# Optimization experiments

Measured on AMD Instinct MI355X. Metric: run time of the kernel, lower is better.

The kernel has to match this reference:

```python
import jax, jax.numpy as jnp
import numpy as np

N_TOKEN = 100000
D = 1024  # d_embed == d_model == d_proj
CUTOFFS = [0, 20000, 60000, 100000]  # cutoff_ends
N_SEQ = 2048


def setup_inputs() -> dict:
    key = jax.random.key(0)
    ks = jax.random.split(key, 20)
    w = lambda k, s: jax.random.normal(k, s, dtype=jnp.float32) * 0.02
    return {
        "x": jax.random.randint(ks[0], (N_SEQ,), 0, N_TOKEN),
        "labels": jax.random.randint(ks[1], (N_SEQ,), 0, N_TOKEN),
        # adaptive embedding tables (d_emb_i = 1024 / 4**i) and projections [d_proj, d_emb_i]
        "emb_w0": w(ks[2], (20000, 1024)),
        "emb_w1": w(ks[3], (40000, 256)),
        "emb_w2": w(ks[4], (40000, 64)),
        "emb_proj0": w(ks[5], (1024, 1024)),
        "emb_proj1": w(ks[6], (1024, 256)),
        "emb_proj2": w(ks[7], (1024, 64)),
        # adaptive softmax output layers + projections
        "out_w0": w(ks[8], (20000, 1024)),
        "out_b0": jnp.zeros((20000,), jnp.float32),
        "out_w1": w(ks[9], (40000, 256)),
        "out_b1": jnp.zeros((40000,), jnp.float32),
        "out_w2": w(ks[10], (40000, 64)),
        "out_b2": jnp.zeros((40000,), jnp.float32),
        "out_proj0": w(ks[11], (1024, 1024)),
        "out_proj1": w(ks[12], (1024, 256)),
        "out_proj2": w(ks[13], (1024, 64)),
        # cluster head tokens (one per tail cluster)
        "cluster_w": w(ks[14], (2, 1024)),
        "cluster_b": jnp.zeros((2,), jnp.float32),
    }


def _forward(x, labels,
             emb_w0, emb_w1, emb_w2, emb_proj0, emb_proj1, emb_proj2,
             out_w0, out_b0, out_w1, out_b1, out_w2, out_b2,
             out_proj0, out_proj1, out_proj2, cluster_w, cluster_b):
    scale = jnp.asarray(D ** 0.5, jnp.float32)
    # AdaptiveEmbedding (div_val>1): per-cluster embed -> project to d_proj, scatter by range.
    # Equivalent vectorized form: build the full projected table once, then gather.
    table = jnp.concatenate([
        emb_w0 @ emb_proj0.T,   # [20000, D]
        emb_w1 @ emb_proj1.T,   # [40000, D]
        emb_w2 @ emb_proj2.T,   # [40000, D]
    ], axis=0)                   # [N_TOKEN, D]
    hidden = table[x] * scale    # [N, D]

    n = hidden.shape[0]
    rows = jnp.arange(n)

    # Head: cluster-0 vocab + one logit per tail cluster.
    head_w = jnp.concatenate([out_w0, cluster_w], axis=0)   # [20002, D]
    head_b = jnp.concatenate([out_b0, cluster_b], axis=0)   # [20002]
    head_logit = (hidden @ out_proj0) @ head_w.T + head_b   # [N, 20002]
    head_lp = jax.nn.log_softmax(head_logit, axis=-1)
    head_size = head_lp.shape[1]

    # Cluster 0: direct lookup in the head.
    lp0 = head_lp[rows, jnp.clip(labels, 0, CUTOFFS[1] - 1)]

    # Tail clusters: dense per-cluster log-softmax, gathered at shifted target,
    # plus the head cluster-token logprob (original TXL uses column -i).
    def tail(w, b, proj, i):
        l, r = CUTOFFS[i], CUTOFFS[i + 1]
        tail_lp = jax.nn.log_softmax((hidden @ proj) @ w.T + b, axis=-1)  # [N, r-l]
        t = jnp.clip(labels - l, 0, r - l - 1)
        return head_lp[:, head_size - i] + tail_lp[rows, t]

    lp1 = tail(out_w1, out_b1, out_proj1, 1)
    lp2 = tail(out_w2, out_b2, out_proj2, 2)

    logprob = jnp.where(labels < CUTOFFS[1], lp0,
               jnp.where(labels < CUTOFFS[2], lp1, lp2))
    return -logprob  # nll, [N]


def reference(x, labels,
              emb_w0, emb_w1, emb_w2, emb_proj0, emb_proj1, emb_proj2,
              out_w0, out_b0, out_w1, out_b1, out_w2, out_b2,
              out_proj0, out_proj1, out_proj2, cluster_w, cluster_b):
    return _forward(x, labels,
                    emb_w0, emb_w1, emb_w2, emb_proj0, emb_proj1, emb_proj2,
                    out_w0, out_b0, out_w1, out_b1, out_w2, out_b2,
                    out_proj0, out_proj1, out_proj2, cluster_w, cluster_b)
```

## Files before the change

### kernel.cpp

```cpp
#include <hip/hip_runtime.h>

typedef _Float16 f16x8 __attribute__((ext_vector_type(8)));
typedef _Float16 f16x4 __attribute__((ext_vector_type(4)));
typedef float f32x4 __attribute__((ext_vector_type(4)));
typedef int i32x4 __attribute__((ext_vector_type(4)));
typedef int i32x8 __attribute__((ext_vector_type(8)));
typedef unsigned char u8;

#define DEVI __device__ __forceinline__

constexpr int NROWS = 2048;
constexpr int HEADV = 20002;
constexpr int HEADP = 20480;
constexpr int NCBH  = 160;
constexpr int VT    = 40000;
constexpr int VTP   = 40320;
constexpr int NCBT  = 315;

DEVI void glds16(const void* g, void* l) {
  __builtin_amdgcn_global_load_lds((const __attribute__((address_space(1))) unsigned int*)g,
                                   (__attribute__((address_space(3))) unsigned int*)l,
                                   16, 0, 0);
}

#define SIG(r) ((r) & 7)
DEVI int swzb(int b, int r) {
  return (b & ~127) | ((((b >> 4) & 7) ^ SIG(r)) << 4) | (b & 15);
}

DEVI unsigned int to_e4m3(float f) {
  unsigned u = __float_as_uint(f);
  unsigned s = (u >> 24) & 0x80u;
  float a = fabsf(f);
  if (!(a < 448.f)) return s | 0x7E;
  if (a < 0.00097656f) return s;
  int exp = (int)((u >> 23) & 0xFF) - 127;
  int qexp = exp < -6 ? -6 : exp;
  int n = __float2int_rn(a * exp2f((float)(3 - qexp)));
  if (n >= 16) { qexp++; n = 8; }
  return s | (unsigned)(n < 8 ? n : (((qexp + 7) << 3) | (n - 8)));
}

DEVI float fr8(unsigned b) {
  unsigned e = (b >> 3) & 15u, m = b & 7u;
  float v;
  if (e) v = __uint_as_float(((e + 120u) << 23) | (m << 20));
  else   v = (float)m * 0.001953125f;
  return (b & 0x80u) ? -v : v;
}

__global__ void prep_par(const int* __restrict__ x, const int* __restrict__ labels,
                         int* cl, int* headcol, int* tailpos, int* pos1, int* pos2,
                         int* L1, int* L2, int* T0, int* T1, int* T2, int* counts)
{
  int n = blockIdx.x * 256 + threadIdx.x;
  int l = labels[n];
  int c = l < 20000 ? 0 : (l < 60000 ? 1 : 2);
  cl[n] = c;
  headcol[n] = c == 0 ? l : (c == 1 ? 20001 : 20000);
  tailpos[n] = c == 1 ? l - 20000 : (c == 2 ? l - 60000 : 0);
  if (c == 1) { int s = atomicAdd(&counts[0], 1); pos1[n] = s; L1[s] = n; }
  else if (c == 2) { int s = atomicAdd(&counts[1], 1); pos2[n] = s; L2[s] = n; }
  int t = x[n];
  int tc = t < 20000 ? 0 : (t < 60000 ? 1 : 2);
  int s = atomicAdd(&counts[2 + tc], 1);
  (tc == 0 ? T0 : tc == 1 ? T1 : T2)[s] = n;
}

constexpr int PB_A = HEADP * 1024 / 8 / 256;
constexpr int PB_B = PB_A + VTP * 256 / 8 / 256;
constexpr int PB_C = PB_B + VTP * 128 / 8 / 256;
constexpr int PB_D = PB_C + 1024;
constexpr int PB_E = PB_D + 256;
constexpr int PB_F = PB_E + 64;
constexpr int PB_G = PB_F + 1024;
constexpr int PB_H = PB_G + 256;
constexpr int PB_I = PB_H + 128;

DEVI void cvt_f16(const float* src, _Float16* dst, int vb, int tid) {
  int g = vb * 256 + tid;
  float4 v = *(const float4*)(src + (size_t)g * 4);
  f16x4 o = {(_Float16)v.x, (_Float16)v.y, (_Float16)v.z, (_Float16)v.w};
  *(f16x4*)(dst + (size_t)g * 4) = o;
}

DEVI void tr32(const float* in, _Float16* out, int C, int bx, int by, int tid) {
  __shared__ float tile[32][33];
  int c0 = bx * 32, r0 = by * 32;
  int tx = tid & 31, ty = tid >> 5;
  for (int i = 0; i < 4; i++) {
    int c = c0 + tx; int r = r0 + ty + i * 8;
    tile[ty + i * 8][tx] = (c < C) ? in[(size_t)r * C + c] : 0.f;
  }
  __syncthreads();
  for (int i = 0; i < 4; i++)
    out[(size_t)(c0 + ty + i * 8) * 1024 + r0 + tx] = (_Float16)tile[tx][ty + i * 8];
}

DEVI unsigned long pack8(const float* v) {
  unsigned long p = 0;
  #pragma unroll
  for (int j = 0; j < 8; j++) p |= (unsigned long)to_e4m3(v[j] * 64.f) << (8 * j);
  return p;
}

__global__ void fused_pack(const float* __restrict__ out_w0, const float* __restrict__ out_b0,
                           const float* __restrict__ cluster_w, const float* __restrict__ cluster_b,
                           const float* __restrict__ out_w1, const float* __restrict__ out_b1,
                           const float* __restrict__ out_w2, const float* __restrict__ out_b2,
                           const float* __restrict__ emb_proj0, const float* __restrict__ emb_proj1,
                           const float* __restrict__ emb_proj2,
                           const float* __restrict__ out_proj0, const float* __restrict__ out_proj1,
                           const float* __restrict__ out_proj2,
                           u8* headw, float* headb,
                           u8* w1q, float* b1p, u8* w2q, float* b2p,
                           _Float16* ep0f, _Float16* ep1f, _Float16* ep2f,
                           _Float16* op0T, _Float16* op1T, _Float16* op2T,
                           int* lists, int* counts)
{
  int bid = blockIdx.x, tid = threadIdx.x;
  int zi = bid * 256 + tid;
  if (zi < 5 * 2048) lists[zi] = 0;
  if (bid == 41 && tid < 8) counts[tid] = 0;
  if (bid < PB_A) {
    int g = bid * 256 + tid;
    int r = g >> 7, sl = g & 127;
    float v[8] = {};
    if (r < 20000) {
      *(float4*)v = *(const float4*)(out_w0 + (size_t)r * 1024 + sl * 8);
      *(float4*)(v + 4) = *(const float4*)(out_w0 + (size_t)r * 1024 + sl * 8 + 4);
    } else if (r < 20002) {
      *(float4*)v = *(const float4*)(cluster_w + (size_t)(r - 20000) * 1024 + sl * 8);
      *(float4*)(v + 4) = *(const float4*)(cluster_w + (size_t)(r - 20000) * 1024 + sl * 8 + 4);
    }
    *(unsigned long*)(headw + (size_t)r * 1024 + swzb(sl * 8, r)) = pack8(v);
    if (g < HEADP) headb[g] = g < 20000 ? out_b0[g] : (g < HEADV ? cluster_b[g - 20000] : -1e30f);
  } else if (bid < PB_B) {
    int g = (bid - PB_A) * 256 + tid;
    int r = g >> 5, sl = g & 31;
    float v[8] = {};
    if (r < VT) {
      *(float4*)v = *(const float4*)(out_w1 + (size_t)r * 256 + sl * 8);
      *(float4*)(v + 4) = *(const float4*)(out_w1 + (size_t)r * 256 + sl * 8 + 4);
    }
    *(unsigned long*)(w1q + (size_t)r * 256 + swzb(sl * 8, r)) = pack8(v);
    if (g < VTP) b1p[g] = g < VT ? out_b1[g] : -1e30f;
  } else if (bid < PB_C) {
    int g = (bid - PB_B) * 256 + tid;
    int r = g >> 4, sl = g & 15;
    float v[8] = {};
    if (r < VT && sl < 8) {
      *(float4*)v = *(const float4*)(out_w2 + (size_t)r * 64 + sl * 8);
      *(float4*)(v + 4) = *(const float4*)(out_w2 + (size_t)r * 64 + sl * 8 + 4);
    }
    *(unsigned long*)(w2q + (size_t)r * 128 + swzb(sl * 8, r)) = pack8(v);
    if (g < VTP) b2p[g] = g < VT ? out_b2[g] : -1e30f;
  } else if (bid < PB_D) { cvt_f16(emb_proj0, ep0f, bid - PB_C, tid); }
  else if (bid < PB_E) { cvt_f16(emb_proj1, ep1f, bid - PB_D, tid); }
  else if (bid < PB_F) { cvt_f16(emb_proj2, ep2f, bid - PB_E, tid); }
  else if (bid < PB_G) { int l = bid - PB_F; tr32(out_proj0, op0T, 1024, l & 31, l >> 5, tid); }
  else if (bid < PB_H) { int l = bid - PB_G; tr32(out_proj1, op1T, 256, l & 7, l >> 3, tid); }
  else                 { int l = bid - PB_H; tr32(out_proj2, op2T, 64, l & 3, l >> 2, tid); }
}

DEVI void gat(const float* emb, const int* x, const int* list, _Float16* dst,
              int tbase, int vmax, int log2E, int vb, int tid) {
  int g = vb * 256 + tid;
  int r = g >> (log2E - 2);
  int e4 = (g & ((1 << (log2E - 2)) - 1)) << 2;
  int n = list[r];
  int tl = x[n] - tbase;
  tl = tl < 0 ? 0 : (tl >= vmax ? vmax - 1 : tl);
  float4 v = *(const float4*)(emb + ((size_t)tl << log2E) + e4);
  f16x4 o = {(_Float16)(v.x * 32.f), (_Float16)(v.y * 32.f),
             (_Float16)(v.z * 32.f), (_Float16)(v.w * 32.f)};
  *(f16x4*)(dst + ((size_t)r << log2E) + e4) = o;
}

__global__ void fused_gather(const float* __restrict__ emb_w0, const float* __restrict__ emb_w1,
                             const float* __restrict__ emb_w2, const int* __restrict__ x,
                             const int* __restrict__ T0, const int* __restrict__ T1,
                             const int* __restrict__ T2,
                             _Float16* E0, _Float16* E1, _Float16* E2)
{
  int bid = blockIdx.x, tid = threadIdx.x;
  if (bid < 2048)      gat(emb_w0, x, T0, E0, 0, 20000, 10, bid, tid);
  else if (bid < 2560) gat(emb_w1, x, T1, E1, 20000, 40000, 8, bid - 2048, tid);
  else                 gat(emb_w2, x, T2, E2, 60000, 40000, 6, bid - 2560, tid);
}

struct Seg128 {
  const _Float16* A; int lda;
  const _Float16* Wm; int ldw;
  _Float16* C; int ldc; int Nvalid;
  u8* Cq; int ldq;
  const int* amap; const int* cmap; const int* cnt;
  int K; int nblk;
};

DEVI void gemm128_body(const Seg128& s, int rb, int cb) {
  int valid = s.cnt ? *s.cnt : NROWS;
  if (rb * 128 >= valid) return;
  __shared__ __attribute__((aligned(16))) _Float16 As[128 * 32];
  __shared__ __attribute__((aligned(16))) _Float16 Ws[128 * 32];
  int tid = threadIdx.x;
  int lane = tid & 63, wid = tid >> 6;
  int wr = wid >> 1, wc = wid & 1;
  int sr = wid * 32 + (lane >> 2);
  int arow0 = rb * 128 + sr, arow1 = arow0 + 16;
  if (s.amap) { arow0 = s.amap[arow0]; arow1 = s.amap[arow1]; }
  int ko = (lane & 3) * 8;
  const _Float16* ag0 = s.A + (size_t)arow0 * s.lda + ko;
  const _Float16* ag1 = s.A + (size_t)arow1 * s.lda + ko;
  const _Float16* wg0 = s.Wm + (size_t)(cb * 128 + sr) * s.ldw + ko;
  const _Float16* wg1 = wg0 + (size_t)16 * s.ldw;
  _Float16* as0 = As + (wid * 32) * 32;
  _Float16* as1 = as0 + 16 * 32;
  _Float16* ws0 = Ws + (wid * 32) * 32;
  _Float16* ws1 = ws0 + 16 * 32;
  f32x4 acc[4][4] = {};
  int lr = lane & 15, lk = (lane >> 4) * 8;
  const int nk = s.K >> 5;
  for (int kt = 0; kt < nk; ++kt) {
    int kofs = kt * 32;
    glds16(ag0 + kofs, as0);
    glds16(ag1 + kofs, as1);
    glds16(wg0 + kofs, ws0);
    glds16(wg1 + kofs, ws1);
    __syncthreads();
    f16x8 af[4], bf[4];
    #pragma unroll
    for (int mi = 0; mi < 4; mi++)
      af[mi] = *(const f16x8*)(As + (wr * 64 + mi * 16 + lr) * 32 + lk);
    #pragma unroll
    for (int ni = 0; ni < 4; ni++)
      bf[ni] = *(const f16x8*)(Ws + (wc * 64 + ni * 16 + lr) * 32 + lk);
    #pragma unroll
    for (int mi = 0; mi < 4; mi++)
      #pragma unroll
      for (int ni = 0; ni < 4; ni++)
        acc[mi][ni] = __builtin_amdgcn_mfma_f32_16x16x32_f16(af[mi], bf[ni], acc[mi][ni], 0, 0, 0);
    __syncthreads();
  }
  #pragma unroll
  for (int mi = 0; mi < 4; mi++) {
    #pragma unroll
    for (int j = 0; j < 4; j++) {
      int rl = wr * 64 + mi * 16 + (lane >> 4) * 4 + j;
      int rg = rb * 128 + rl;
      if (rg >= valid) continue;
      int orow = s.cmap ? s.cmap[rg] : rg;
      #pragma unroll
      for (int ni = 0; ni < 4; ni++) {
        int col = cb * 128 + wc * 64 + ni * 16 + (lane & 15);
        if (col < s.Nvalid) {
          float v = acc[mi][ni][j];
          s.C[(size_t)orow * s.ldc + col] = (_Float16)v;
          if (s.Cq) s.Cq[(size_t)orow * s.ldq + swzb(col, orow)] = (u8)to_e4m3(v * 8.f);
        }
      }
    }
  }
}

__global__ __launch_bounds__(256)
void gemm128_multi(Seg128 s0, Seg128 s1, Seg128 s2) {
  int b = blockIdx.x;
  if (b < s0.nblk)                    { gemm128_body(s0, b & 15, b >> 4); }
  else if (b < s0.nblk + s1.nblk)     { b -= s0.nblk; gemm128_body(s1, b & 15, b >> 4); }
  else                                { b -= s0.nblk + s1.nblk; gemm128_body(s2, b & 15, b >> 4); }
}

struct SegL {
  const u8* A; const u8* W; const float* bias; const int* cnt;
  float* pm; float* ps; int K; int nblk;
};

__global__ __launch_bounds__(256, 2)
void gemm_lse8_multi(SegL s0, SegL s1, SegL s2)
{
  __shared__ __attribute__((aligned(16))) u8 As[32768];
  __shared__ __attribute__((aligned(16))) u8 Ws[16384];

  int b = blockIdx.x;
  SegL s;
  if (b < s0.nblk) s = s0;
  else if (b < s0.nblk + s1.nblk) { s = s1; b -= s0.nblk; }
  else { s = s2; b -= s0.nblk + s1.nblk; }

  int q = s.nblk >> 3;
  int w = (b & 7) * q + (b >> 3);
  int rb = w & 7, cb = w >> 3;
  int valid = s.cnt ? *s.cnt : NROWS;
  if (rb * 256 >= valid) return;

  const int K = s.K;
  int tid = threadIdx.x;
  int lane = tid & 63, wid = tid >> 6;
  int lr = lane & 15, g = lane >> 4;

  const u8* aS[8]; int dA[8];
  #pragma unroll
  for (int i = 0; i < 8; ++i) {
    int c = tid + i * 256;
    aS[i] = s.A + (size_t)(rb * 256 + (c >> 3)) * K + (c & 7) * 16;
    dA[i] = c * 16;
  }
  const u8* bS[4]; int dB[4];
  #pragma unroll
  for (int i = 0; i < 4; ++i) {
    int c = tid + i * 256;
    bS[i] = s.W + (size_t)((size_t)cb * 128 + (c >> 3)) * K + (c & 7) * 16;
    dB[i] = c * 16;
  }

  int sig = SIG(lr);
  int p0 = ((2 * g + 0) ^ sig) << 4;
  int p1 = ((2 * g + 1) ^ sig) << 4;
  int arow = (wid * 64 + lr) * 128;
  int brow = lr * 128;

  f32x4 acc[4][8] = {};
  const int nk = K >> 7;

  union UV { i32x8 v; i32x4 h[2]; };
  for (int kt = 0; kt < nk; ++kt) {
    int k0 = kt * 128;
    #pragma unroll
    for (int i = 0; i < 8; ++i) glds16(aS[i] + k0, As + dA[i]);
    #pragma unroll
    for (int i = 0; i < 4; ++i) glds16(bS[i] + k0, Ws + dB[i]);
    __syncthreads();
    i32x8 bq[8];
    #pragma unroll
    for (int ni = 0; ni < 8; ++ni) {
      UV bv;
      const u8* bp = Ws + brow + ni * 2048;
      bv.h[0] = *(const i32x4*)(bp + p0);
      bv.h[1] = *(const i32x4*)(bp + p1);
      bq[ni] = bv.v;
    }
    #pragma unroll
    for (int mi = 0; mi < 4; ++mi) {
      UV av;
      const u8* ap = As + arow + mi * 2048;
      av.h[0] = *(const i32x4*)(ap + p0);
      av.h[1] = *(const i32x4*)(ap + p1);
      #pragma unroll
      for (int ni = 0; ni < 8; ++ni)
        acc[mi][ni] = __builtin_amdgcn_mfma_scale_f32_16x16x128_f8f6f4(
                        av.v, bq[ni], acc[mi][ni], 0, 0, 0, 127, 0, 127);
    }
    __syncthreads();
  }

  float bv8[8];
  #pragma unroll
  for (int ni = 0; ni < 8; ++ni) bv8[ni] = s.bias[cb * 128 + ni * 16 + lr];
  constexpr float INV = 1.f / 512.f;
  #pragma unroll
  for (int mi = 0; mi < 4; ++mi) {
    #pragma unroll
    for (int j = 0; j < 4; ++j) {
      float vv[8]; float m = -3e38f;
      #pragma unroll
      for (int ni = 0; ni < 8; ++ni) {
        vv[ni] = acc[mi][ni][j] * INV + bv8[ni];
        m = fmaxf(m, vv[ni]);
      }
      #pragma unroll
      for (int d = 1; d < 16; d <<= 1) m = fmaxf(m, __shfl_xor(m, d));
      float sm = 0.f;
      #pragma unroll
      for (int ni = 0; ni < 8; ++ni) sm += __expf(vv[ni] - m);
      #pragma unroll
      for (int d = 1; d < 16; d <<= 1) sm += __shfl_xor(sm, d);
      if (lr == 0) {
        int row = rb * 256 + wid * 64 + mi * 16 + g * 4 + j;
        s.pm[(size_t)cb * 2048 + row] = m;
        s.ps[(size_t)cb * 2048 + row] = sm;
      }
    }
  }
}

DEVI float lsew(const float* m, const float* s, int nb, int lane) {
  float M = -3e38f;
  for (int i = lane; i < nb; i += 64) M = fmaxf(M, m[(size_t)i * 2048]);
  #pragma unroll
  for (int d = 1; d < 64; d <<= 1) M = fmaxf(M, __shfl_xor(M, d));
  float S = 0.f;
  for (int i = lane; i < nb; i += 64) S += s[(size_t)i * 2048] * __expf(m[(size_t)i * 2048] - M);
  #pragma unroll
  for (int d = 1; d < 64; d <<= 1) S += __shfl_xor(S, d);
  return M + __logf(S);
}

__global__ void finish_kernel(const _Float16* __restrict__ ph0, const u8* __restrict__ headw,
                              const float* __restrict__ headb,
                              const _Float16* __restrict__ ph1c, const u8* __restrict__ w1q,
                              const float* __restrict__ b1p,
                              const _Float16* __restrict__ ph2c, const u8* __restrict__ w2q,
                              const float* __restrict__ b2p,
                              const int* __restrict__ headcol, const int* __restrict__ tailpos,
                              const int* __restrict__ pos1, const int* __restrict__ pos2,
                              const int* __restrict__ cl,
                              const float* __restrict__ pmh, const float* __restrict__ psh,
                              const float* __restrict__ pm1, const float* __restrict__ ps1,
                              const float* __restrict__ pm2, const float* __restrict__ ps2,
                              float* __restrict__ out)
{
  int n = blockIdx.x;
  int tid = threadIdx.x, lane = tid & 63, wid = tid >> 6;
  __shared__ float sh[6];
  int c = cl[n];
  constexpr float IW = 1.f / 64.f;
  if (wid == 0) {
    int hc = headcol[n];
    const f16x8* a = (const f16x8*)(ph0 + (size_t)n * 1024 + lane * 16);
    float s = 0.f;
    #pragma unroll
    for (int u = 0; u < 2; u++) {
      unsigned long wq = *(const unsigned long*)(headw + (size_t)hc * 1024 + swzb(lane * 16 + u * 8, hc));
      f16x8 av = a[u];
      #pragma unroll
      for (int j = 0; j < 8; j++) s += (float)av[j] * fr8((unsigned)(wq >> (8 * j)) & 0xFFu);
    }
    #pragma unroll
    for (int d = 1; d < 64; d <<= 1) s += __shfl_xor(s, d);
    if (lane == 0) sh[0] = s * IW + headb[hc];
  } else if (wid == 1 && c == 1) {
    int p = pos1[n], t = tailpos[n];
    f16x4 av = *(const f16x4*)(ph1c + (size_t)p * 256 + lane * 4);
    const u8* ww = w1q + (size_t)t * 256 + swzb(lane * 4, t);
    float s = (float)av[0] * fr8(ww[0]) + (float)av[1] * fr8(ww[1])
            + (float)av[2] * fr8(ww[2]) + (float)av[3] * fr8(ww[3]);
    #pragma unroll
    for (int d = 1; d < 64; d <<= 1) s += __shfl_xor(s, d);
    float l = lsew(pm1 + p, ps1 + p, NCBT, lane);
    if (lane == 0) { sh[1] = s * IW + b1p[t]; sh[4] = l; }
  } else if (wid == 2 && c == 2) {
    int p = pos2[n], t = tailpos[n];
    const _Float16* a = ph2c + (size_t)p * 128 + lane * 2;
    const u8* ww = w2q + (size_t)t * 128 + swzb(lane * 2, t);
    float s = (float)a[0] * fr8(ww[0]) + (float)a[1] * fr8(ww[1]);
    #pragma unroll
    for (int d = 1; d < 64; d <<= 1) s += __shfl_xor(s, d);
    float l = lsew(pm2 + p, ps2 + p, NCBT, lane);
    if (lane == 0) { sh[2] = s * IW + b2p[t]; sh[5] = l; }
  } else if (wid == 3) {
    float l = lsew(pmh + n, psh + n, NCBH, lane);
    if (lane == 0) sh[3] = l;
  }
  __syncthreads();
  if (tid == 0) {
    float nll = sh[3] - sh[0];
    if (c == 1)      nll += sh[4] - sh[1];
    else if (c == 2) nll += sh[5] - sh[2];
    out[n] = nll;
  }
}

extern "C" void kernel_launch(void* const* d_in, const int* in_sizes, int n_in,
                              void* d_out, int out_size, void* d_ws, size_t ws_size,
                              hipStream_t stream)
{
  const int*   x         = (const int*)d_in[0];
  const int*   labels    = (const int*)d_in[1];
  const float* emb_w0    = (const float*)d_in[2];
  const float* emb_w1    = (const float*)d_in[3];
  const float* emb_w2    = (const float*)d_in[4];
  const float* emb_proj0 = (const float*)d_in[5];
  const float* emb_proj1 = (const float*)d_in[6];
  const float* emb_proj2 = (const float*)d_in[7];
  const float* out_w0    = (const float*)d_in[8];
  const float* out_b0    = (const float*)d_in[9];
  const float* out_w1    = (const float*)d_in[10];
  const float* out_b1    = (const float*)d_in[11];
  const float* out_w2    = (const float*)d_in[12];
  const float* out_b2    = (const float*)d_in[13];
  const float* out_proj0 = (const float*)d_in[14];
  const float* out_proj1 = (const float*)d_in[15];
  const float* out_proj2 = (const float*)d_in[16];
  const float* cluster_w = (const float*)d_in[17];
  const float* cluster_b = (const float*)d_in[18];
  float* out = (float*)d_out;

  char* ws = (char*)d_ws;
  size_t off = 0;
  auto alloc = [&](size_t bytes) -> void* {
    void* p = ws + off;
    off = (off + bytes + 255) & ~(size_t)255;
    return p;
  };
  u8*    headw = (u8*)alloc((size_t)HEADP * 1024);
  float* headb = (float*)alloc((size_t)HEADP * 4);
  u8*    w1q   = (u8*)alloc((size_t)VTP * 256);
  float* b1p   = (float*)alloc((size_t)VTP * 4);
  u8*    w2q   = (u8*)alloc((size_t)VTP * 128);
  float* b2p   = (float*)alloc((size_t)VTP * 4);
  _Float16* ep0f = (_Float16*)alloc((size_t)1024 * 1024 * 2);
  _Float16* ep1f = (_Float16*)alloc((size_t)1024 * 256 * 2);
  _Float16* ep2f = (_Float16*)alloc((size_t)1024 * 64 * 2);
  _Float16* op0T = (_Float16*)alloc((size_t)1024 * 1024 * 2);
  _Float16* op1T = (_Float16*)alloc((size_t)256 * 1024 * 2);
  _Float16* op2T = (_Float16*)alloc((size_t)128 * 1024 * 2);
  _Float16* E0   = (_Float16*)alloc((size_t)NROWS * 1024 * 2);
  _Float16* E1   = (_Float16*)alloc((size_t)NROWS * 256 * 2);
  _Float16* E2   = (_Float16*)alloc((size_t)NROWS * 64 * 2);
  _Float16* hid  = (_Float16*)alloc((size_t)NROWS * 1024 * 2);
  _Float16* ph0  = (_Float16*)alloc((size_t)NROWS * 1024 * 2);
  u8*       ph0q = (u8*)alloc((size_t)NROWS * 1024);
  _Float16* ph1c = (_Float16*)alloc((size_t)NROWS * 256 * 2);
  u8*       ph1q = (u8*)alloc((size_t)NROWS * 256);
  _Float16* ph2c = (_Float16*)alloc((size_t)NROWS * 128 * 2);
  u8*       ph2q = (u8*)alloc((size_t)NROWS * 128);
  float* pmh = (float*)alloc((size_t)NCBH * 2048 * 4);
  float* psh = (float*)alloc((size_t)NCBH * 2048 * 4);
  float* pm1 = (float*)alloc((size_t)NCBT * 2048 * 4);
  float* ps1 = (float*)alloc((size_t)NCBT * 2048 * 4);
  float* pm2 = (float*)alloc((size_t)NCBT * 2048 * 4);
  float* ps2 = (float*)alloc((size_t)NCBT * 2048 * 4);
  int* lists = (int*)alloc(5 * NROWS * 4);
  int* L1 = lists;
  int* L2 = lists + 2048;
  int* T0 = lists + 4096;
  int* T1 = lists + 6144;
  int* T2 = lists + 8192;
  int* counts  = (int*)alloc(16 * 4);
  int* cl      = (int*)alloc(NROWS * 4);
  int* headcol = (int*)alloc(NROWS * 4);
  int* tailpos = (int*)alloc(NROWS * 4);
  int* pos1    = (int*)alloc(NROWS * 4);
  int* pos2    = (int*)alloc(NROWS * 4);
  (void)ws_size; (void)in_sizes; (void)n_in; (void)out_size;

  fused_pack<<<PB_I, 256, 0, stream>>>(out_w0, out_b0, cluster_w, cluster_b,
                                       out_w1, out_b1, out_w2, out_b2,
                                       emb_proj0, emb_proj1, emb_proj2,
                                       out_proj0, out_proj1, out_proj2,
                                       headw, headb, w1q, b1p, w2q, b2p,
                                       ep0f, ep1f, ep2f, op0T, op1T, op2T,
                                       lists, counts);

  prep_par<<<8, 256, 0, stream>>>(x, labels, cl, headcol, tailpos, pos1, pos2,
                                  L1, L2, T0, T1, T2, counts);

  fused_gather<<<2688, 256, 0, stream>>>(emb_w0, emb_w1, emb_w2, x, T0, T1, T2, E0, E1, E2);

  Seg128 h0 = {E0, 1024, ep0f, 1024, hid, 1024, 1024, nullptr, 0, nullptr, T0, counts + 2, 1024, 128};
  Seg128 h1 = {E1, 256,  ep1f, 256,  hid, 1024, 1024, nullptr, 0, nullptr, T1, counts + 3, 256,  128};
  Seg128 h2 = {E2, 64,   ep2f, 64,   hid, 1024, 1024, nullptr, 0, nullptr, T2, counts + 4, 64,   128};
  gemm128_multi<<<384, 256, 0, stream>>>(h0, h1, h2);

  Seg128 p0 = {hid, 1024, op0T, 1024, ph0,  1024, 1024, ph0q, 1024, nullptr, nullptr, nullptr,   1024, 128};
  Seg128 p1 = {hid, 1024, op1T, 1024, ph1c, 256,  256,  ph1q, 256,  L1,      nullptr, counts + 0, 1024, 32};
  Seg128 p2 = {hid, 1024, op2T, 1024, ph2c, 128,  128,  ph2q, 128,  L2,      nullptr, counts + 1, 1024, 16};
  gemm128_multi<<<176, 256, 0, stream>>>(p0, p1, p2);

  SegL l0 = {ph0q, headw, headb, nullptr,    pmh, psh, 1024, 8 * NCBH};
  SegL l1 = {ph1q, w1q,   b1p,   counts + 0, pm1, ps1, 256,  8 * NCBT};
  SegL l2 = {ph2q, w2q,   b2p,   counts + 1, pm2, ps2, 128,  8 * NCBT};
  gemm_lse8_multi<<<8 * NCBH + 16 * NCBT, 256, 0, stream>>>(l0, l1, l2);

  finish_kernel<<<NROWS, 256, 0, stream>>>(ph0, headw, headb, ph1c, w1q, b1p,
                                           ph2c, w2q, b2p, headcol, tailpos, pos1, pos2, cl,
                                           pmh, psh, pm1, ps1, pm2, ps2, out);
}
```

Before: 252.1 us.

## Double-buffer LDS in FP8 LSE GEMM to overlap loads with MFMA

Converts the gemm_lse8_multi main loop from a single-buffered load, sync, compute, sync pattern into a two-stage LDS ping-pong. The next K tile is prefetched with global_load_lds while the current tile is consumed, using explicit vmcnt waits, sched barriers and s_setprio around the MFMA section. The aim is to hide global-memory latency behind matrix math. LDS use doubles to 96 KB, so launch bounds drop to one block per SIMD group, which lowers occupancy. Trailing iterations redundantly reload the last tile.

```diff
diff --git a/kernel.cpp b/kernel.cpp
--- a/kernel.cpp
+++ b/kernel.cpp
@@ -22,6 +22,12 @@
                                    (__attribute__((address_space(3))) unsigned int*)l,
                                    16, 0, 0);
 }
+
+#define VMW(N) asm volatile("s_waitcnt vmcnt(" #N ")" ::: "memory")
+#define SCB    __builtin_amdgcn_sched_barrier(0)
+#define BARR   __builtin_amdgcn_s_barrier()
+#define PR1 __builtin_amdgcn_s_setprio(1)
+#define PR0 __builtin_amdgcn_s_setprio(0)
 
 #define SIG(r) ((r) & 7)
 DEVI int swzb(int b, int r) {
@@ -276,11 +282,11 @@
   float* pm; float* ps; int K; int nblk;
 };
 
-__global__ __launch_bounds__(256, 2)
+__global__ __launch_bounds__(256, 1)
 void gemm_lse8_multi(SegL s0, SegL s1, SegL s2)
 {
-  __shared__ __attribute__((aligned(16))) u8 As[32768];
-  __shared__ __attribute__((aligned(16))) u8 Ws[16384];
+  constexpr int RSZ = 49152;
+  __shared__ __attribute__((aligned(16))) u8 lds[2 * RSZ];
 
   int b = blockIdx.x;
   SegL s;
@@ -311,31 +317,38 @@
   for (int i = 0; i < 4; ++i) {
     int c = tid + i * 256;
     bS[i] = s.W + (size_t)((size_t)cb * 128 + (c >> 3)) * K + (c & 7) * 16;
-    dB[i] = c * 16;
-  }
+    dB[i] = 32768 + c * 16;
+  }
+  auto STAGE = [&](u8* rg, int k0) {
+    #pragma unroll
+    for (int i = 0; i < 8; ++i) glds16(aS[i] + k0, rg + dA[i]);
+    #pragma unroll
+    for (int i = 0; i < 4; ++i) glds16(bS[i] + k0, rg + dB[i]);
+  };
 
   int sig = SIG(lr);
   int p0 = ((2 * g + 0) ^ sig) << 4;
   int p1 = ((2 * g + 1) ^ sig) << 4;
   int arow = (wid * 64 + lr) * 128;
-  int brow = lr * 128;
+  int brow = 32768 + lr * 128;
 
   f32x4 acc[4][8] = {};
   const int nk = K >> 7;
 
+  asm volatile("s_waitcnt vmcnt(0) lgkmcnt(0)" ::: "memory");
+  STAGE(lds, 0);
+  STAGE(lds + RSZ, (nk > 1 ? 1 : 0) * 128);
+  VMW(12); SCB; BARR; SCB;
+
   union UV { i32x8 v; i32x4 h[2]; };
-  for (int kt = 0; kt < nk; ++kt) {
-    int k0 = kt * 128;
-    #pragma unroll
-    for (int i = 0; i < 8; ++i) glds16(aS[i] + k0, As + dA[i]);
-    #pragma unroll
-    for (int i = 0; i < 4; ++i) glds16(bS[i] + k0, Ws + dB[i]);
-    __syncthreads();
+  for (int t = 0; t < nk; ++t) {
+    u8* cur = lds + (t & 1) * RSZ;
+    PR1;
     i32x8 bq[8];
     #pragma unroll
     for (int ni = 0; ni < 8; ++ni) {
       UV bv;
-      const u8* bp = Ws + brow + ni * 2048;
+      const u8* bp = cur + brow + ni * 2048;
       bv.h[0] = *(const i32x4*)(bp + p0);
       bv.h[1] = *(const i32x4*)(bp + p1);
       bq[ni] = bv.v;
@@ -343,7 +356,7 @@
     #pragma unroll
     for (int mi = 0; mi < 4; ++mi) {
       UV av;
-      const u8* ap = As + arow + mi * 2048;
+      const u8* ap = cur + arow + mi * 2048;
       av.h[0] = *(const i32x4*)(ap + p0);
       av.h[1] = *(const i32x4*)(ap + p1);
       #pragma unroll
@@ -351,8 +364,13 @@
         acc[mi][ni] = __builtin_amdgcn_mfma_scale_f32_16x16x128_f8f6f4(
                         av.v, bq[ni], acc[mi][ni], 0, 0, 0, 127, 0, 127);
     }
-    __syncthreads();
-  }
+    PR0;
+    SCB; BARR; SCB;
+    int ts = (t + 2 > nk - 1) ? nk - 1 : t + 2;
+    STAGE(cur, ts * 128);
+    VMW(12); SCB;
+  }
+  VMW(0);
 
   float bv8[8];
   #pragma unroll
```

Result: slower. 337.2 us (+33.8%).
